# Optimization experiments

Measured on AMD Instinct MI355X. Metric: run time of the kernel, lower is better.

The kernel has to match this reference:

```python
import jax, jax.numpy as jnp
import numpy as np

N_NODES = 100000
N_EDGES = 3200000
IN_DIM = 128


def setup_inputs() -> dict:
    key = jax.random.key(0)
    ks = jax.random.split(key, 6)
    x = jax.random.normal(ks[0], (N_NODES, IN_DIM), dtype=jnp.float32)
    edge_index = jax.random.randint(ks[1], (2, N_EDGES), 0, N_NODES, dtype=jnp.int64)
    # Glorot-ish init for weights, zero bias (PyG GCNConv default has bias)
    W1 = jax.random.normal(ks[2], (IN_DIM, 32), dtype=jnp.float32) / np.sqrt(IN_DIM)
    b1 = jnp.zeros((32,), dtype=jnp.float32)
    W2 = jax.random.normal(ks[3], (32, 16), dtype=jnp.float32) / np.sqrt(32.0)
    b2 = jnp.zeros((16,), dtype=jnp.float32)
    Wf = jax.random.normal(ks[4], (16, 1), dtype=jnp.float32) / np.sqrt(16.0)
    bf = jnp.zeros((1,), dtype=jnp.float32)
    return {"x": x, "edge_index": edge_index, "W1": W1, "b1": b1,
            "W2": W2, "b2": b2, "Wf": Wf, "bf": bf}


def reference(x, edge_index, W1, b1, W2, b2, Wf, bf):
    N = x.shape[0]
    # PyG GCNConv: add self-loops, symmetric normalization D^-1/2 (A+I) D^-1/2
    loop = jnp.arange(N, dtype=edge_index.dtype)
    src = jnp.concatenate([edge_index[0], loop])  # message sources (x_j)
    dst = jnp.concatenate([edge_index[1], loop])  # aggregation targets
    deg = jax.ops.segment_sum(jnp.ones_like(dst, dtype=x.dtype), dst, num_segments=N)
    dinv = jax.lax.rsqrt(jnp.maximum(deg, 1.0))  # deg >= 1 due to self-loops
    norm = dinv[src] * dinv[dst]                  # per-edge coefficient

    def gcn_conv(h, W, b):
        h = h @ W                                 # linear transform first (small dim)
        msg = h[src] * norm[:, None]              # gather + scale
        return jax.ops.segment_sum(msg, dst, num_segments=N) + b  # scatter-add

    h = jax.nn.relu(gcn_conv(x, W1, b1))
    h = jax.nn.relu(gcn_conv(h, W2, b2))
    return (h @ Wf + bf).squeeze(-1)              # [N]
```

## Files before the change

### kernel.cpp

```cpp
#include <hip/hip_runtime.h>


#define TPB 256
#define NBUCK 256
#define BCAP 16384
#define CHUNK 8192

__device__ __forceinline__ unsigned f2bf(float f) {
    unsigned u = __float_as_uint(f);
    return (u + 0x7FFFu + ((u >> 16) & 1u)) >> 16;
}
__device__ __forceinline__ float bflo(unsigned u) { return __uint_as_float(u << 16); }
__device__ __forceinline__ float bfhi(unsigned u) { return __uint_as_float(u & 0xFFFF0000u); }

__global__ __launch_bounds__(512) void binA2_kernel(
        const int* __restrict__ src, const int* __restrict__ dst,
        int* __restrict__ bcur, unsigned* __restrict__ staging, int E, int NPB) {
    __shared__ unsigned packed[CHUNK];
    __shared__ unsigned char buckb[CHUNK];
    __shared__ int hist[NBUCK];
    __shared__ int scan_[NBUCK];
    __shared__ int lstart[NBUCK];
    __shared__ int lcur[NBUCK];
    __shared__ int gbase[NBUCK];
    int tid = threadIdx.x;
    int start = blockIdx.x * CHUNK;
    int sz = min(CHUNK, E - start);

    if (tid < NBUCK) hist[tid] = 0;
    __syncthreads();
    for (int i = tid; i < sz; i += 512) {
        unsigned d = (unsigned)dst[start + i];
        atomicAdd(&hist[d / (unsigned)NPB], 1);
    }
    __syncthreads();
    int v = (tid < NBUCK) ? hist[tid] : 0;
    if (tid < NBUCK) scan_[tid] = v;
    __syncthreads();
    for (int dd = 1; dd < NBUCK; dd <<= 1) {
        int t = 0;
        if (tid < NBUCK && tid >= dd) t = scan_[tid - dd];
        __syncthreads();
        if (tid < NBUCK) scan_[tid] += t;
        __syncthreads();
    }
    if (tid < NBUCK) {
        lstart[tid] = scan_[tid] - v;
        lcur[tid] = 0;
        gbase[tid] = atomicAdd(&bcur[tid], v);
    }
    __syncthreads();
    for (int i = tid; i < sz; i += 512) {
        unsigned d = (unsigned)dst[start + i];
        unsigned s = (unsigned)src[start + i];
        unsigned b = d / (unsigned)NPB;
        unsigned loc = d - b * (unsigned)NPB;
        int pos = atomicAdd(&lcur[b], 1);
        int si = lstart[b] + pos;
        packed[si] = (loc << 20) | s;
        buckb[si] = (unsigned char)b;
    }
    __syncthreads();
    for (int i = tid; i < sz; i += 512) {
        unsigned b = buckb[i];
        int dsti = gbase[b] + (i - lstart[b]);
        if (dsti < BCAP)
            staging[(size_t)b * BCAP + dsti] = packed[i];
    }
}

__global__ void buildB_kernel(const int* __restrict__ bcur,
                              const unsigned* __restrict__ staging,
                              int* __restrict__ offs, int* __restrict__ counts,
                              float* __restrict__ dinv, int* __restrict__ csr_src,
                              int N, int NPB) {
    __shared__ int sb[NBUCK];
    __shared__ int hist[512];
    __shared__ int scan_[512];
    __shared__ int cur[512];
    int b = blockIdx.x;
    int tid = threadIdx.x;
    if (tid < NBUCK) sb[tid] = min(bcur[tid], BCAP);
    __syncthreads();
    for (int d = 1; d < NBUCK; d <<= 1) {
        int t = 0;
        if (tid < NBUCK && tid >= d) t = sb[tid - d];
        __syncthreads();
        if (tid < NBUCK) sb[tid] += t;
        __syncthreads();
    }
    int sz = min(bcur[b], BCAP);
    int base = (b == 0) ? 0 : sb[b - 1];
    int n0 = b * NPB;
    int nn = min(NPB, N - n0);
    const unsigned* se = staging + (size_t)b * BCAP;

    hist[tid] = 0;
    __syncthreads();
    for (int i = tid; i < sz; i += 512)
        atomicAdd(&hist[se[i] >> 20], 1);
    __syncthreads();
    int h = hist[tid];
    scan_[tid] = h;
    __syncthreads();
    for (int d = 1; d < 512; d <<= 1) {
        int t = 0;
        if (tid >= d) t = scan_[tid - d];
        __syncthreads();
        scan_[tid] += t;
        __syncthreads();
    }
    int excl = scan_[tid] - h;
    cur[tid] = excl;
    if (tid < nn) {
        int node = n0 + tid;
        offs[node] = base + excl;
        counts[node] = h;
        dinv[node] = rsqrtf((float)(h + 1));
    }
    __syncthreads();
    for (int i = tid; i < sz; i += 512) {
        unsigned p = se[i];
        int pos = atomicAdd(&cur[p >> 20], 1);
        csr_src[base + pos] = (int)(p & 0xFFFFFu);
    }
}

__global__ __launch_bounds__(256) void gemm1_kernel(
        const float* __restrict__ x, const float* __restrict__ W1,
        const float* __restrict__ dinv, unsigned* __restrict__ xwd, int N) {
    __shared__ float ws_[128 * 32];
    for (int i = threadIdx.x; i < 128 * 32; i += blockDim.x) ws_[i] = W1[i];
    __syncthreads();
    int t = threadIdx.x;
    int node = blockIdx.x * 64 + (t >> 2);
    if (node >= N) return;
    int jq = (t & 3) * 8;
    float acc[8];
#pragma unroll
    for (int j = 0; j < 8; ++j) acc[j] = 0.0f;
    const float4* xr = (const float4*)(x + (size_t)node * 128);
#pragma unroll 4
    for (int k4 = 0; k4 < 32; ++k4) {
        float4 xv = xr[k4];
        const float* wb = ws_ + (k4 * 4) * 32 + jq;
        float4 a0 = *(const float4*)(wb);
        float4 a1 = *(const float4*)(wb + 4);
        float4 b0 = *(const float4*)(wb + 32);
        float4 b1v = *(const float4*)(wb + 36);
        float4 c0 = *(const float4*)(wb + 64);
        float4 c1 = *(const float4*)(wb + 68);
        float4 d0 = *(const float4*)(wb + 96);
        float4 d1 = *(const float4*)(wb + 100);
        acc[0] += xv.x * a0.x + xv.y * b0.x + xv.z * c0.x + xv.w * d0.x;
        acc[1] += xv.x * a0.y + xv.y * b0.y + xv.z * c0.y + xv.w * d0.y;
        acc[2] += xv.x * a0.z + xv.y * b0.z + xv.z * c0.z + xv.w * d0.z;
        acc[3] += xv.x * a0.w + xv.y * b0.w + xv.z * c0.w + xv.w * d0.w;
        acc[4] += xv.x * a1.x + xv.y * b1v.x + xv.z * c1.x + xv.w * d1.x;
        acc[5] += xv.x * a1.y + xv.y * b1v.y + xv.z * c1.y + xv.w * d1.y;
        acc[6] += xv.x * a1.z + xv.y * b1v.z + xv.z * c1.z + xv.w * d1.z;
        acc[7] += xv.x * a1.w + xv.y * b1v.w + xv.z * c1.w + xv.w * d1.w;
    }
    float d = dinv[node];
    unsigned pk0 = f2bf(acc[0] * d) | (f2bf(acc[1] * d) << 16);
    unsigned pk1 = f2bf(acc[2] * d) | (f2bf(acc[3] * d) << 16);
    unsigned pk2 = f2bf(acc[4] * d) | (f2bf(acc[5] * d) << 16);
    unsigned pk3 = f2bf(acc[6] * d) | (f2bf(acc[7] * d) << 16);
    ((uint4*)(xwd + (size_t)node * 16))[t & 3] = make_uint4(pk0, pk1, pk2, pk3);
}

__global__ __launch_bounds__(256) void aggS32_kernel(
        const int* __restrict__ offs, const int* __restrict__ counts,
        const int* __restrict__ csr_src, const float* __restrict__ dinv,
        const unsigned* __restrict__ xwd, float* __restrict__ agg, int N) {
    int t = threadIdx.x;
    int q = t & 3;
    int node = blockIdx.x * 64 + (t >> 2);
    if (node >= N) return;
    int off = offs[node];
    int deg = counts[node];
    float acc[8];
    {
        uint4 v = ((const uint4*)(xwd + (size_t)node * 16))[q];
        acc[0] = bflo(v.x); acc[1] = bfhi(v.x);
        acc[2] = bflo(v.y); acc[3] = bfhi(v.y);
        acc[4] = bflo(v.z); acc[5] = bfhi(v.z);
        acc[6] = bflo(v.w); acc[7] = bfhi(v.w);
    }
    int i = 0;
    for (; i + 1 < deg; i += 2) {
        int s0 = csr_src[off + i];
        int s1 = csr_src[off + i + 1];
        uint4 v0 = ((const uint4*)(xwd + (size_t)s0 * 16))[q];
        uint4 v1 = ((const uint4*)(xwd + (size_t)s1 * 16))[q];
        acc[0] += bflo(v0.x) + bflo(v1.x); acc[1] += bfhi(v0.x) + bfhi(v1.x);
        acc[2] += bflo(v0.y) + bflo(v1.y); acc[3] += bfhi(v0.y) + bfhi(v1.y);
        acc[4] += bflo(v0.z) + bflo(v1.z); acc[5] += bfhi(v0.z) + bfhi(v1.z);
        acc[6] += bflo(v0.w) + bflo(v1.w); acc[7] += bfhi(v0.w) + bfhi(v1.w);
    }
    if (i < deg) {
        int s = csr_src[off + i];
        uint4 v = ((const uint4*)(xwd + (size_t)s * 16))[q];
        acc[0] += bflo(v.x); acc[1] += bfhi(v.x);
        acc[2] += bflo(v.y); acc[3] += bfhi(v.y);
        acc[4] += bflo(v.z); acc[5] += bfhi(v.z);
        acc[6] += bflo(v.w); acc[7] += bfhi(v.w);
    }
    float dv = dinv[node];
    float* op = agg + (size_t)node * 32 + q * 8;
    ((float4*)op)[0] = make_float4(acc[0] * dv, acc[1] * dv, acc[2] * dv, acc[3] * dv);
    ((float4*)op)[1] = make_float4(acc[4] * dv, acc[5] * dv, acc[6] * dv, acc[7] * dv);
}

__global__ void gemm2_kernel(const float* __restrict__ agg1, const float* __restrict__ W2,
                             const float* __restrict__ b1, const float* __restrict__ dinv,
                             unsigned* __restrict__ h2wd, int N) {
    __shared__ float ws_[32 * 16];
    __shared__ float bs_[32];
    for (int i = threadIdx.x; i < 32 * 16; i += blockDim.x) ws_[i] = W2[i];
    if (threadIdx.x < 32) bs_[threadIdx.x] = b1[threadIdx.x];
    __syncthreads();
    int node = blockIdx.x * blockDim.x + threadIdx.x;
    if (node >= N) return;
    float h[32];
    const float4* ar = (const float4*)(agg1 + (size_t)node * 32);
#pragma unroll
    for (int k4 = 0; k4 < 8; ++k4) {
        float4 v = ar[k4];
        h[k4 * 4 + 0] = fmaxf(v.x + bs_[k4 * 4 + 0], 0.0f);
        h[k4 * 4 + 1] = fmaxf(v.y + bs_[k4 * 4 + 1], 0.0f);
        h[k4 * 4 + 2] = fmaxf(v.z + bs_[k4 * 4 + 2], 0.0f);
        h[k4 * 4 + 3] = fmaxf(v.w + bs_[k4 * 4 + 3], 0.0f);
    }
    float acc[16];
#pragma unroll
    for (int j = 0; j < 16; ++j) acc[j] = 0.0f;
#pragma unroll
    for (int k = 0; k < 32; ++k) {
        float hv = h[k];
#pragma unroll
        for (int j4 = 0; j4 < 4; ++j4) {
            float4 w = *(const float4*)(ws_ + k * 16 + j4 * 4);
            acc[j4 * 4 + 0] += hv * w.x;
            acc[j4 * 4 + 1] += hv * w.y;
            acc[j4 * 4 + 2] += hv * w.z;
            acc[j4 * 4 + 3] += hv * w.w;
        }
    }
    float d = dinv[node];
    unsigned pk[8];
#pragma unroll
    for (int j = 0; j < 8; ++j)
        pk[j] = f2bf(acc[2 * j] * d) | (f2bf(acc[2 * j + 1] * d) << 16);
    uint4* hp = (uint4*)(h2wd + (size_t)node * 8);
    hp[0] = make_uint4(pk[0], pk[1], pk[2], pk[3]);
    hp[1] = make_uint4(pk[4], pk[5], pk[6], pk[7]);
}

__global__ __launch_bounds__(256) void aggS16f_kernel(
        const int* __restrict__ offs, const int* __restrict__ counts,
        const int* __restrict__ csr_src, const float* __restrict__ dinv,
        const unsigned* __restrict__ h2wd,
        const float* __restrict__ b2, const float* __restrict__ Wf,
        const float* __restrict__ bf, float* __restrict__ out, int N) {
    __shared__ float bs_[16];
    __shared__ float wf_[16];
    __shared__ float bfv;
    int t = threadIdx.x;
    if (t < 16) { bs_[t] = b2[t]; wf_[t] = Wf[t]; }
    if (t == 0) bfv = bf[0];
    __syncthreads();
    int q = t & 1;
    int node = blockIdx.x * 128 + (t >> 1);
    if (node >= N) return;
    int off = offs[node];
    int deg = counts[node];
    float acc[8];
    {
        uint4 v = ((const uint4*)(h2wd + (size_t)node * 8))[q];
        acc[0] = bflo(v.x); acc[1] = bfhi(v.x);
        acc[2] = bflo(v.y); acc[3] = bfhi(v.y);
        acc[4] = bflo(v.z); acc[5] = bfhi(v.z);
        acc[6] = bflo(v.w); acc[7] = bfhi(v.w);
    }
    int i = 0;
    for (; i + 1 < deg; i += 2) {
        int s0 = csr_src[off + i];
        int s1 = csr_src[off + i + 1];
        uint4 v0 = ((const uint4*)(h2wd + (size_t)s0 * 8))[q];
        uint4 v1 = ((const uint4*)(h2wd + (size_t)s1 * 8))[q];
        acc[0] += bflo(v0.x) + bflo(v1.x); acc[1] += bfhi(v0.x) + bfhi(v1.x);
        acc[2] += bflo(v0.y) + bflo(v1.y); acc[3] += bfhi(v0.y) + bfhi(v1.y);
        acc[4] += bflo(v0.z) + bflo(v1.z); acc[5] += bfhi(v0.z) + bfhi(v1.z);
        acc[6] += bflo(v0.w) + bflo(v1.w); acc[7] += bfhi(v0.w) + bfhi(v1.w);
    }
    if (i < deg) {
        int s = csr_src[off + i];
        uint4 v = ((const uint4*)(h2wd + (size_t)s * 8))[q];
        acc[0] += bflo(v.x); acc[1] += bfhi(v.x);
        acc[2] += bflo(v.y); acc[3] += bfhi(v.y);
        acc[4] += bflo(v.z); acc[5] += bfhi(v.z);
        acc[6] += bflo(v.w); acc[7] += bfhi(v.w);
    }
    float dv = dinv[node];
    const float* bq = bs_ + q * 8;
    const float* wq = wf_ + q * 8;
    float part = 0.f;
#pragma unroll
    for (int k = 0; k < 8; ++k)
        part += fmaxf(acc[k] * dv + bq[k], 0.f) * wq[k];
    part += __shfl_xor(part, 1, 64);
    if (q == 0) out[node] = part + bfv;
}

extern "C" void kernel_launch(void* const* d_in, const int* in_sizes, int n_in,
                              void* d_out, int out_size, void* d_ws, size_t ws_size,
                              hipStream_t stream) {
    const float* x  = (const float*)d_in[0];
    const int*   ei = (const int*)d_in[1];
    const float* W1 = (const float*)d_in[2];
    const float* b1 = (const float*)d_in[3];
    const float* W2 = (const float*)d_in[4];
    const float* b2 = (const float*)d_in[5];
    const float* Wf = (const float*)d_in[6];
    const float* bf = (const float*)d_in[7];

    int N = in_sizes[0] / 128;
    int E = in_sizes[1] / 2;
    const int* src = ei;
    const int* dst = ei + E;
    int NPB = (N + NBUCK - 1) / NBUCK;

    size_t Np = ((size_t)N + 3) & ~(size_t)3;
    size_t Ep = ((size_t)E + 3) & ~(size_t)3;
    int* wsI      = (int*)d_ws;
    int* counts   = wsI;
    int* offs     = counts + Np;
    int* bcur     = offs + Np;
    int* csr_src  = bcur + NBUCK;
    float* dinv   = (float*)(csr_src + Ep);
    unsigned* xwd = (unsigned*)(dinv + Np);
    float* agg1   = (float*)(xwd + 16 * Np);
    unsigned* h2wd= (unsigned*)(agg1 + 32 * Np);
    float* out    = (float*)d_out;
    unsigned* staging = (unsigned*)agg1;

    int nbG1 = (N + 63) / 64;
    int nbC  = (E + CHUNK - 1) / CHUNK;
    int nbN  = (N + TPB - 1) / TPB;
    int nbA32 = (N + 63) / 64;
    int nbA16 = (N + 127) / 128;

    hipMemsetAsync(bcur, 0, NBUCK * sizeof(int), stream);
    binA2_kernel<<<nbC, 512, 0, stream>>>(src, dst, bcur, staging, E, NPB);
    buildB_kernel<<<NBUCK, 512, 0, stream>>>(bcur, staging, offs, counts,
                                             dinv, csr_src, N, NPB);
    gemm1_kernel<<<nbG1, 256, 0, stream>>>(x, W1, dinv, xwd, N);
    aggS32_kernel<<<nbA32, 256, 0, stream>>>(offs, counts, csr_src, dinv, xwd, agg1, N);
    gemm2_kernel<<<nbN, TPB, 0, stream>>>(agg1, W2, b1, dinv, h2wd, N);
    aggS16f_kernel<<<nbA16, 256, 0, stream>>>(offs, counts, csr_src, dinv, h2wd,
                                              b2, Wf, bf, out, N);
}
```

Before: 272.3 us.

## Fuse layer-1 aggregation with second GEMM, register-block gemm1, double bucket count

Fuses the first aggregation kernel with the 32x16 transform. Each quad of threads applies bias and ReLU to its 8 features, forms partial products with W2 held in shared memory, and reduces them with cross-lane shuffles before writing the bf16 layer-2 input. This removes the fp32 agg1 round trip through global memory and one kernel launch. gemm1 now handles 4 nodes per thread to reuse shared-memory weight loads, and the binning uses 512 buckets with half the per-bucket capacity, which shrinks the staging area but risks overflow if any bucket exceeds 8192 edges.

```diff
diff --git a/kernel.cpp b/kernel.cpp
--- a/kernel.cpp
+++ b/kernel.cpp
@@ -2,8 +2,8 @@
 
 
 #define TPB 256
-#define NBUCK 256
-#define BCAP 16384
+#define NBUCK 512
+#define BCAP 8192
 #define CHUNK 8192
 
 __device__ __forceinline__ unsigned f2bf(float f) {
@@ -17,7 +17,7 @@
         const int* __restrict__ src, const int* __restrict__ dst,
         int* __restrict__ bcur, unsigned* __restrict__ staging, int E, int NPB) {
     __shared__ unsigned packed[CHUNK];
-    __shared__ unsigned char buckb[CHUNK];
+    __shared__ unsigned short buckb[CHUNK];
     __shared__ int hist[NBUCK];
     __shared__ int scan_[NBUCK];
     __shared__ int lstart[NBUCK];
@@ -58,7 +58,7 @@
         int pos = atomicAdd(&lcur[b], 1);
         int si = lstart[b] + pos;
         packed[si] = (loc << 20) | s;
-        buckb[si] = (unsigned char)b;
+        buckb[si] = (unsigned short)b;
     }
     __syncthreads();
     for (int i = tid; i < sz; i += 512) {
@@ -130,19 +130,27 @@
         const float* __restrict__ x, const float* __restrict__ W1,
         const float* __restrict__ dinv, unsigned* __restrict__ xwd, int N) {
     __shared__ float ws_[128 * 32];
-    for (int i = threadIdx.x; i < 128 * 32; i += blockDim.x) ws_[i] = W1[i];
+    for (int i = threadIdx.x; i < 128 * 32; i += 256) ws_[i] = W1[i];
     __syncthreads();
     int t = threadIdx.x;
-    int node = blockIdx.x * 64 + (t >> 2);
-    if (node >= N) return;
     int jq = (t & 3) * 8;
-    float acc[8];
-#pragma unroll
-    for (int j = 0; j < 8; ++j) acc[j] = 0.0f;
-    const float4* xr = (const float4*)(x + (size_t)node * 128);
-#pragma unroll 4
+    int n0 = blockIdx.x * 256 + (t >> 2) * 4;
+    if (n0 >= N) return;
+    int nc0 = min(n0 + 0, N - 1);
+    int nc1 = min(n0 + 1, N - 1);
+    int nc2 = min(n0 + 2, N - 1);
+    int nc3 = min(n0 + 3, N - 1);
+    const float4* xr0 = (const float4*)(x + (size_t)nc0 * 128);
+    const float4* xr1 = (const float4*)(x + (size_t)nc1 * 128);
+    const float4* xr2 = (const float4*)(x + (size_t)nc2 * 128);
+    const float4* xr3 = (const float4*)(x + (size_t)nc3 * 128);
+    float acc[4][8];
+#pragma unroll
+    for (int n = 0; n < 4; ++n)
+#pragma unroll
+        for (int j = 0; j < 8; ++j) acc[n][j] = 0.0f;
+#pragma unroll 2
     for (int k4 = 0; k4 < 32; ++k4) {
-        float4 xv = xr[k4];
         const float* wb = ws_ + (k4 * 4) * 32 + jq;
         float4 a0 = *(const float4*)(wb);
         float4 a1 = *(const float4*)(wb + 4);
@@ -152,27 +160,44 @@
         float4 c1 = *(const float4*)(wb + 68);
         float4 d0 = *(const float4*)(wb + 96);
         float4 d1 = *(const float4*)(wb + 100);
-        acc[0] += xv.x * a0.x + xv.y * b0.x + xv.z * c0.x + xv.w * d0.x;
-        acc[1] += xv.x * a0.y + xv.y * b0.y + xv.z * c0.y + xv.w * d0.y;
-        acc[2] += xv.x * a0.z + xv.y * b0.z + xv.z * c0.z + xv.w * d0.z;
-        acc[3] += xv.x * a0.w + xv.y * b0.w + xv.z * c0.w + xv.w * d0.w;
-        acc[4] += xv.x * a1.x + xv.y * b1v.x + xv.z * c1.x + xv.w * d1.x;
-        acc[5] += xv.x * a1.y + xv.y * b1v.y + xv.z * c1.y + xv.w * d1.y;
-        acc[6] += xv.x * a1.z + xv.y * b1v.z + xv.z * c1.z + xv.w * d1.z;
-        acc[7] += xv.x * a1.w + xv.y * b1v.w + xv.z * c1.w + xv.w * d1.w;
-    }
-    float d = dinv[node];
-    unsigned pk0 = f2bf(acc[0] * d) | (f2bf(acc[1] * d) << 16);
-    unsigned pk1 = f2bf(acc[2] * d) | (f2bf(acc[3] * d) << 16);
-    unsigned pk2 = f2bf(acc[4] * d) | (f2bf(acc[5] * d) << 16);
-    unsigned pk3 = f2bf(acc[6] * d) | (f2bf(acc[7] * d) << 16);
-    ((uint4*)(xwd + (size_t)node * 16))[t & 3] = make_uint4(pk0, pk1, pk2, pk3);
-}
-
-__global__ __launch_bounds__(256) void aggS32_kernel(
+        float4 xv0 = xr0[k4];
+        float4 xv1 = xr1[k4];
+        float4 xv2 = xr2[k4];
+        float4 xv3 = xr3[k4];
+#pragma unroll
+        for (int n = 0; n < 4; ++n) {
+            float4 xv = (n == 0) ? xv0 : (n == 1) ? xv1 : (n == 2) ? xv2 : xv3;
+            acc[n][0] += xv.x * a0.x + xv.y * b0.x + xv.z * c0.x + xv.w * d0.x;
+            acc[n][1] += xv.x * a0.y + xv.y * b0.y + xv.z * c0.y + xv.w * d0.y;
+            acc[n][2] += xv.x * a0.z + xv.y * b0.z + xv.z * c0.z + xv.w * d0.z;
+            acc[n][3] += xv.x * a0.w + xv.y * b0.w + xv.z * c0.w + xv.w * d0.w;
+            acc[n][4] += xv.x * a1.x + xv.y * b1v.x + xv.z * c1.x + xv.w * d1.x;
+            acc[n][5] += xv.x * a1.y + xv.y * b1v.y + xv.z * c1.y + xv.w * d1.y;
+            acc[n][6] += xv.x * a1.z + xv.y * b1v.z + xv.z * c1.z + xv.w * d1.z;
+            acc[n][7] += xv.x * a1.w + xv.y * b1v.w + xv.z * c1.w + xv.w * d1.w;
+        }
+    }
+#pragma unroll
+    for (int n = 0; n < 4; ++n) {
+        int node = n0 + n;
+        if (node >= N) break;
+        float d = dinv[node];
+        unsigned pk0 = f2bf(acc[n][0] * d) | (f2bf(acc[n][1] * d) << 16);
+        unsigned pk1 = f2bf(acc[n][2] * d) | (f2bf(acc[n][3] * d) << 16);
+        unsigned pk2 = f2bf(acc[n][4] * d) | (f2bf(acc[n][5] * d) << 16);
+        unsigned pk3 = f2bf(acc[n][6] * d) | (f2bf(acc[n][7] * d) << 16);
+        ((uint4*)(xwd + (size_t)node * 16))[t & 3] = make_uint4(pk0, pk1, pk2, pk3);
+    }
+}
+
+__global__ __launch_bounds__(256) void aggF_kernel(
         const int* __restrict__ offs, const int* __restrict__ counts,
         const int* __restrict__ csr_src, const float* __restrict__ dinv,
-        const unsigned* __restrict__ xwd, float* __restrict__ agg, int N) {
+        const unsigned* __restrict__ xwd, const float* __restrict__ b1,
+        const float* __restrict__ W2, unsigned* __restrict__ h2wd, int N) {
+    __shared__ float ws2[32 * 16];
+    for (int i = threadIdx.x; i < 512; i += 256) ws2[i] = W2[i];
+    __syncthreads();
     int t = threadIdx.x;
     int q = t & 3;
     int node = blockIdx.x * 64 + (t >> 2);
@@ -207,54 +232,41 @@
         acc[6] += bflo(v.w); acc[7] += bfhi(v.w);
     }
     float dv = dinv[node];
-    float* op = agg + (size_t)node * 32 + q * 8;
-    ((float4*)op)[0] = make_float4(acc[0] * dv, acc[1] * dv, acc[2] * dv, acc[3] * dv);
-    ((float4*)op)[1] = make_float4(acc[4] * dv, acc[5] * dv, acc[6] * dv, acc[7] * dv);
-}
-
-__global__ void gemm2_kernel(const float* __restrict__ agg1, const float* __restrict__ W2,
-                             const float* __restrict__ b1, const float* __restrict__ dinv,
-                             unsigned* __restrict__ h2wd, int N) {
-    __shared__ float ws_[32 * 16];
-    __shared__ float bs_[32];
-    for (int i = threadIdx.x; i < 32 * 16; i += blockDim.x) ws_[i] = W2[i];
-    if (threadIdx.x < 32) bs_[threadIdx.x] = b1[threadIdx.x];
-    __syncthreads();
-    int node = blockIdx.x * blockDim.x + threadIdx.x;
-    if (node >= N) return;
-    float h[32];
-    const float4* ar = (const float4*)(agg1 + (size_t)node * 32);
-#pragma unroll
-    for (int k4 = 0; k4 < 8; ++k4) {
-        float4 v = ar[k4];
-        h[k4 * 4 + 0] = fmaxf(v.x + bs_[k4 * 4 + 0], 0.0f);
-        h[k4 * 4 + 1] = fmaxf(v.y + bs_[k4 * 4 + 1], 0.0f);
-        h[k4 * 4 + 2] = fmaxf(v.z + bs_[k4 * 4 + 2], 0.0f);
-        h[k4 * 4 + 3] = fmaxf(v.w + bs_[k4 * 4 + 3], 0.0f);
-    }
-    float acc[16];
-#pragma unroll
-    for (int j = 0; j < 16; ++j) acc[j] = 0.0f;
-#pragma unroll
-    for (int k = 0; k < 32; ++k) {
-        float hv = h[k];
-#pragma unroll
-        for (int j4 = 0; j4 < 4; ++j4) {
-            float4 w = *(const float4*)(ws_ + k * 16 + j4 * 4);
-            acc[j4 * 4 + 0] += hv * w.x;
-            acc[j4 * 4 + 1] += hv * w.y;
-            acc[j4 * 4 + 2] += hv * w.z;
-            acc[j4 * 4 + 3] += hv * w.w;
-        }
-    }
-    float d = dinv[node];
-    unsigned pk[8];
-#pragma unroll
-    for (int j = 0; j < 8; ++j)
-        pk[j] = f2bf(acc[2 * j] * d) | (f2bf(acc[2 * j + 1] * d) << 16);
-    uint4* hp = (uint4*)(h2wd + (size_t)node * 8);
-    hp[0] = make_uint4(pk[0], pk[1], pk[2], pk[3]);
-    hp[1] = make_uint4(pk[4], pk[5], pk[6], pk[7]);
+    float part[16];
+#pragma unroll
+    for (int j = 0; j < 16; ++j) part[j] = 0.0f;
+    const float* bq = b1 + q * 8;
+#pragma unroll
+    for (int k = 0; k < 8; ++k) {
+        float h = fmaxf(acc[k] * dv + bq[k], 0.0f);
+        const float* wr = ws2 + (q * 8 + k) * 16;
+        float4 w0 = *(const float4*)(wr);
+        float4 w1 = *(const float4*)(wr + 4);
+        float4 w2 = *(const float4*)(wr + 8);
+        float4 w3 = *(const float4*)(wr + 12);
+        part[0]  += h * w0.x; part[1]  += h * w0.y; part[2]  += h * w0.z; part[3]  += h * w0.w;
+        part[4]  += h * w1.x; part[5]  += h * w1.y; part[6]  += h * w1.z; part[7]  += h * w1.w;
+        part[8]  += h * w2.x; part[9]  += h * w2.y; part[10] += h * w2.z; part[11] += h * w2.w;
+        part[12] += h * w3.x; part[13] += h * w3.y; part[14] += h * w3.z; part[15] += h * w3.w;
+    }
+    float p8[8];
+#pragma unroll
+    for (int j = 0; j < 8; ++j) {
+        float send = (q & 1) ? part[j] : part[j + 8];
+        float keep = (q & 1) ? part[j + 8] : part[j];
+        p8[j] = keep + __shfl_xor(send, 1, 64);
+    }
+    float p4[4];
+#pragma unroll
+    for (int j = 0; j < 4; ++j) {
+        float send = (q & 2) ? p8[j] : p8[j + 4];
+        float keep = (q & 2) ? p8[j + 4] : p8[j];
+        p4[j] = keep + __shfl_xor(send, 2, 64);
+    }
+    unsigned pk0 = f2bf(p4[0] * dv) | (f2bf(p4[1] * dv) << 16);
+    unsigned pk1 = f2bf(p4[2] * dv) | (f2bf(p4[3] * dv) << 16);
+    int slot = ((q & 1) << 1) | ((q >> 1) & 1);
+    ((uint2*)(h2wd + (size_t)node * 8))[slot] = make_uint2(pk0, pk1);
 }
 
 __global__ __launch_bounds__(256) void aggS16f_kernel(
@@ -340,14 +352,12 @@
     int* csr_src  = bcur + NBUCK;
     float* dinv   = (float*)(csr_src + Ep);
     unsigned* xwd = (unsigned*)(dinv + Np);
-    float* agg1   = (float*)(xwd + 16 * Np);
-    unsigned* h2wd= (unsigned*)(agg1 + 32 * Np);
+    unsigned* staging = xwd + 16 * Np;
+    unsigned* h2wd = staging;
     float* out    = (float*)d_out;
-    unsigned* staging = (unsigned*)agg1;
-
-    int nbG1 = (N + 63) / 64;
+
+    int nbG1 = (N + 255) / 256;
     int nbC  = (E + CHUNK - 1) / CHUNK;
-    int nbN  = (N + TPB - 1) / TPB;
     int nbA32 = (N + 63) / 64;
     int nbA16 = (N + 127) / 128;
 
@@ -356,8 +366,8 @@
     buildB_kernel<<<NBUCK, 512, 0, stream>>>(bcur, staging, offs, counts,
                                              dinv, csr_src, N, NPB);
     gemm1_kernel<<<nbG1, 256, 0, stream>>>(x, W1, dinv, xwd, N);
-    aggS32_kernel<<<nbA32, 256, 0, stream>>>(offs, counts, csr_src, dinv, xwd, agg1, N);
-    gemm2_kernel<<<nbN, TPB, 0, stream>>>(agg1, W2, b1, dinv, h2wd, N);
+    aggF_kernel<<<nbA32, 256, 0, stream>>>(offs, counts, csr_src, dinv, xwd,
+                                           b1, W2, h2wd, N);
     aggS16f_kernel<<<nbA16, 256, 0, stream>>>(offs, counts, csr_src, dinv, h2wd,
                                               b2, Wf, bf, out, N);
 }
```

After: 259.6 us. 1.05x faster.
